# Optimization experiments

Hardware: AMD Instinct MI355X
Metric: run time of the kernel (lower is better)

Reference implementation:

```python
import jax, jax.numpy as jnp
import numpy as np

# Config mirroring the torch module's __init__ args
B = 2
LQ = 2048      # length_q
LKV = 2048     # length_kv
H = 8          # head_num
DQK = 64       # dim_QK
DV = 64        # dim_V
DIM_Q = 512
DIM_K = 512
DIM_VIN = 512
DIM_OUT = 512
SPAN = 64
STRIDE = 1


def setup_inputs() -> dict:
    key = jax.random.key(0)
    ks = jax.random.split(key, 7)
    s = 0.02  # small init scale for weights
    return {
        "q": jax.random.normal(ks[0], (B, LQ, DIM_Q), jnp.float32),
        "k": jax.random.normal(ks[1], (B, LKV, DIM_K), jnp.float32),
        "v": jax.random.normal(ks[2], (B, LKV, DIM_VIN), jnp.float32),
        "Wq": jax.random.normal(ks[3], (DIM_Q, H * DQK), jnp.float32) * s,
        "Wk": jax.random.normal(ks[4], (DIM_K, H * DQK), jnp.float32) * s,
        "Wv": jax.random.normal(ks[5], (DIM_VIN, H * DV), jnp.float32) * s,
        "Wout": jax.random.normal(ks[6], (H * DV, DIM_OUT), jnp.float32) * s,
    }


def reference(q, k, v, Wq, Wk, Wv, Wout):
    # Projections (torch nn.Linear without bias; weights stored as [in, out] here)
    Q = (q @ Wq).reshape(B, LQ, H, DQK)    # [B, Lq, H, DQK]
    K = (k @ Wk).reshape(B, LKV, H, DQK)   # [B, Lkv, H, DQK]
    V = (v @ Wv).reshape(B, LKV, H, DV)    # [B, Lkv, H, DV]

    # Window index table: for query t, key slot s attends kv position
    # kvi[s, t] = s - (SPAN-1) + STRIDE*t   (the conv1d-unfold in the original)
    s_idx = jnp.arange(SPAN)[:, None]
    t_idx = jnp.arange(LQ)[None, :]
    kvi = s_idx - (SPAN - 1) + STRIDE * t_idx          # [span, Lq]
    valid = (kvi >= 0) & (kvi < LKV)                   # [span, Lq]
    idx = jnp.clip(kvi, 0, LKV - 1)

    # Gather sliding windows (equivalent to conv_K/conv_V im2col tables)
    Kw = K[:, idx]   # [B, span, Lq, H, DQK]
    Vw = V[:, idx]   # [B, span, Lq, H, DV]

    scale = jnp.asarray(1.0 / np.sqrt(DQK), jnp.float32)
    scores = jnp.einsum('bthd,bsthd->bhst', Q, Kw) * scale   # [B, H, span, Lq]
    scores = jnp.where(valid[None, None], scores, -jnp.inf)
    p = jax.nn.softmax(scores, axis=2)                        # softmax over span

    o = jnp.einsum('bhst,bsthd->bthd', p, Vw).reshape(B, LQ, H * DV)
    return o @ Wout   # [B, Lq, dim_out]
```

## Files before the change

### kernel.cpp

```cpp
#include <hip/hip_runtime.h>

#define NB 2
#define SEQ 2048
#define NH 8
#define HD 64
#define DMODEL 512
#define WSPAN 64
#define MROWS (NB * SEQ)

typedef __attribute__((ext_vector_type(4))) float f32x4;
typedef __attribute__((ext_vector_type(4))) int i32x4;
typedef __attribute__((ext_vector_type(8))) short bf16x8;

static __device__ __forceinline__ float bf2f(unsigned short u) {
    return __uint_as_float(((unsigned int)u) << 16);
}
static __device__ __forceinline__ unsigned short f2bf(float f) {
    unsigned int x = __float_as_uint(f);
    x += 0x7fffu + ((x >> 16) & 1u);
    return (unsigned short)(x >> 16);
}

static __device__ __forceinline__ f32x4 mfma16(bf16x8 a, bf16x8 b, f32x4 c) {
    return __builtin_amdgcn_mfma_f32_16x16x32_bf16(a, b, c, 0, 0, 0);
}

struct Cvt3 {
    const float* src[3];
    unsigned short* dst[3];
};

__global__ __launch_bounds__(256) void cvt_big(Cvt3 a) {
    const int ai = blockIdx.y;
    const int idx = blockIdx.x * 256 + threadIdx.x;
    const float* s = a.src[ai] + (size_t)idx * 8;
    float4 f0 = *(const float4*)s;
    float4 f1 = *(const float4*)(s + 4);
    i32x4 o;
    o[0] = (int)((unsigned)f2bf(f0.x) | ((unsigned)f2bf(f0.y) << 16));
    o[1] = (int)((unsigned)f2bf(f0.z) | ((unsigned)f2bf(f0.w) << 16));
    o[2] = (int)((unsigned)f2bf(f1.x) | ((unsigned)f2bf(f1.y) << 16));
    o[3] = (int)((unsigned)f2bf(f1.z) | ((unsigned)f2bf(f1.w) << 16));
    *(i32x4*)(a.dst[ai] + (size_t)idx * 8) = o;
}

struct Wt4 {
    const float* src[4];
    unsigned short* dst[4];
};

__global__ __launch_bounds__(256) void cvt_wT(Wt4 a) {
    __shared__ unsigned short t64[64][72];
    const int w = blockIdx.z;
    const float* src = a.src[w];
    unsigned short* dst = a.dst[w];
    const int k0 = blockIdx.x * 64, n0 = blockIdx.y * 64;
    const int t = threadIdx.x;
    const int r = t >> 2;
    const int cg = (t & 3) * 16;
    const float* sp = src + (size_t)(k0 + r) * DMODEL + n0 + cg;
#pragma unroll
    for (int j = 0; j < 16; j += 4) {
        float4 f = *(const float4*)(sp + j);
        t64[r][cg + j + 0] = f2bf(f.x);
        t64[r][cg + j + 1] = f2bf(f.y);
        t64[r][cg + j + 2] = f2bf(f.z);
        t64[r][cg + j + 3] = f2bf(f.w);
    }
    __syncthreads();
    unsigned short buf[16];
#pragma unroll
    for (int j = 0; j < 16; ++j) buf[j] = t64[cg + j][r];
    unsigned short* dp = dst + (size_t)(n0 + r) * DMODEL + k0 + cg;
    *(i32x4*)dp = *(const i32x4*)buf;
    *(i32x4*)(dp + 8) = *(const i32x4*)(buf + 8);
}

#define TBM 128
#define TBN 128
#define TBK 32
#define LPAD 40

template <bool OUT_F32>
static __device__ __forceinline__ void gemm_core(const unsigned short* __restrict__ A,
                                                 const unsigned short* __restrict__ BT,
                                                 void* __restrict__ C, int m0, int n0) {
    constexpr int N = DMODEL, K = DMODEL;
    __shared__ __align__(16) unsigned short a_lds[TBM][LPAD];
    __shared__ __align__(16) unsigned short b_lds[TBN][LPAD];
    const int t = threadIdx.x;
    const int lane = t & 63;
    const int wv = t >> 6;
    const int s_r = t >> 1;
    const int s_k = (t & 1) * 16;
    const int fr = lane & 15;
    const int fk = (lane >> 4) * 8;
    const int wm = (wv & 1) * 64;
    const int wn = (wv >> 1) * 64;

    f32x4 acc[4][4];
#pragma unroll
    for (int i = 0; i < 4; ++i)
#pragma unroll
        for (int j = 0; j < 4; ++j) acc[i][j] = (f32x4){0.f, 0.f, 0.f, 0.f};

    for (int k0 = 0; k0 < K; k0 += TBK) {
        const unsigned short* ap = A + (size_t)(m0 + s_r) * K + k0 + s_k;
        const unsigned short* bp = BT + (size_t)(n0 + s_r) * K + k0 + s_k;
        i32x4 av0 = *(const i32x4*)ap;
        i32x4 av1 = *(const i32x4*)(ap + 8);
        i32x4 bv0 = *(const i32x4*)bp;
        i32x4 bv1 = *(const i32x4*)(bp + 8);
        __syncthreads();
        *(i32x4*)&a_lds[s_r][s_k] = av0;
        *(i32x4*)&a_lds[s_r][s_k + 8] = av1;
        *(i32x4*)&b_lds[s_r][s_k] = bv0;
        *(i32x4*)&b_lds[s_r][s_k + 8] = bv1;
        __syncthreads();
        bf16x8 af[4], bf[4];
#pragma unroll
        for (int i = 0; i < 4; ++i) {
            af[i] = *(const bf16x8*)&a_lds[wm + i * 16 + fr][fk];
            bf[i] = *(const bf16x8*)&b_lds[wn + i * 16 + fr][fk];
        }
#pragma unroll
        for (int mi = 0; mi < 4; ++mi)
#pragma unroll
            for (int ni = 0; ni < 4; ++ni) acc[mi][ni] = mfma16(af[mi], bf[ni], acc[mi][ni]);
    }
#pragma unroll
    for (int mi = 0; mi < 4; ++mi) {
#pragma unroll
        for (int ni = 0; ni < 4; ++ni) {
#pragma unroll
            for (int r = 0; r < 4; ++r) {
                const int row = m0 + wm + mi * 16 + (lane >> 4) * 4 + r;
                const int col = n0 + wn + ni * 16 + fr;
                if constexpr (OUT_F32)
                    ((float*)C)[(size_t)row * N + col] = acc[mi][ni][r];
                else
                    ((unsigned short*)C)[(size_t)row * N + col] = f2bf(acc[mi][ni][r]);
            }
        }
    }
}

__global__ __launch_bounds__(256) void gemm_proj(
    const unsigned short* __restrict__ qx, const unsigned short* __restrict__ kx,
    const unsigned short* __restrict__ vx, const unsigned short* __restrict__ wtq,
    const unsigned short* __restrict__ wtk, const unsigned short* __restrict__ wtv,
    unsigned short* __restrict__ Qp, unsigned short* __restrict__ Kp,
    unsigned short* __restrict__ Vp) {
    const unsigned short* A;
    const unsigned short* W;
    unsigned short* C;
    if (blockIdx.z == 0) { A = qx; W = wtq; C = Qp; }
    else if (blockIdx.z == 1) { A = kx; W = wtk; C = Kp; }
    else { A = vx; W = wtv; C = Vp; }
    gemm_core<false>(A, W, C, blockIdx.x * TBM, blockIdx.y * TBN);
}

__global__ __launch_bounds__(256) void gemm_out(const unsigned short* __restrict__ Op,
                                                const unsigned short* __restrict__ wto,
                                                float* __restrict__ out) {
    gemm_core<true>(Op, wto, out, blockIdx.x * TBM, blockIdx.y * TBN);
}

__global__ __launch_bounds__(256) void attn_win(const unsigned short* __restrict__ Qp,
                                                const unsigned short* __restrict__ Kp,
                                                const unsigned short* __restrict__ Vp,
                                                unsigned short* __restrict__ Op) {
    __shared__ __align__(16) unsigned short kt[128 * 64];
    __shared__ __align__(16) unsigned short vT[64 * 128];
    __shared__ __align__(16) unsigned short pw[4][16][104];
    const int tile = blockIdx.x, h = blockIdx.y, b = blockIdx.z;
    const int t0 = tile * 64;
    const int tid = threadIdx.x;
    const int lane = tid & 63;
    const int qg = tid >> 6;
    const int c = lane & 15;
    const int g = lane >> 4;
    const int hcol = h * HD;
    const size_t base = (size_t)b * SEQ * DMODEL;

    {
        const int l = tid >> 1;
        const int dh = (tid & 1) * 32;
        int j = t0 - (WSPAN - 1) + l;
        int jc = j < 0 ? 0 : (j > SEQ - 1 ? SEQ - 1 : j);
        const unsigned short* kp = Kp + base + (size_t)jc * DMODEL + hcol + dh;
        const unsigned short* vp = Vp + base + (size_t)jc * DMODEL + hcol + dh;
        const int lg = (l & 7) << 4;
#pragma unroll
        for (int u = 0; u < 4; ++u) {
            const int dg = dh + u * 8;
            i32x4 kv = *(const i32x4*)(kp + u * 8);
            i32x4 vv = *(const i32x4*)(vp + u * 8);
            *(i32x4*)((char*)kt + l * 128 + ((dg * 2) ^ lg)) = kv;
#pragma unroll
            for (int e2 = 0; e2 < 4; ++e2) {
                unsigned int w2 = (unsigned int)vv[e2];
                const int d0 = dg + 2 * e2, d1 = d0 + 1;
                *(unsigned short*)((char*)vT + d0 * 256 + ((((l >> 3) ^ (d0 & 15)) << 4)) +
                                   (l & 7) * 2) = (unsigned short)(w2 & 0xffffu);
                *(unsigned short*)((char*)vT + d1 * 256 + ((((l >> 3) ^ (d1 & 15)) << 4)) +
                                   (l & 7) * 2) = (unsigned short)(w2 >> 16);
            }
        }
    }
    *(unsigned long long*)&pw[qg][lane >> 2][80 + (lane & 3) * 4] = 0ull;
    __syncthreads();

    const unsigned short* qrow =
        Qp + base + (size_t)(t0 + 16 * qg + c) * DMODEL + hcol + 8 * g;
    const bf16x8 qa0 = *(const bf16x8*)qrow;
    const bf16x8 qa1 = *(const bf16x8*)(qrow + 32);
    f32x4 sacc[5];
#pragma unroll
    for (int kb = 0; kb < 5; ++kb) {
        sacc[kb] = (f32x4){0.f, 0.f, 0.f, 0.f};
        const int key = 16 * (qg + kb) + c;
        const int sw = (key & 7) << 4;
        bf16x8 kf0 = *(const bf16x8*)((const char*)kt + key * 128 + ((16 * g) ^ sw));
        bf16x8 kf1 = *(const bf16x8*)((const char*)kt + key * 128 + ((64 + 16 * g) ^ sw));
        sacc[kb] = mfma16(qa0, kf0, sacc[kb]);
        sacc[kb] = mfma16(qa1, kf1, sacc[kb]);
    }

    const int L0 = 63 - t0;
#pragma unroll
    for (int r = 0; r < 4; ++r) {
        const int iq = 4 * g + r;
        float sv[5];
        float m = -3e38f;
#pragma unroll
        for (int kb = 0; kb < 5; ++kb) {
            float x = sacc[kb][r] * 0.125f;
            const int dlk = 16 * kb + c - iq;
            const int l = 16 * (qg + kb) + c;
            x = (dlk >= 0 && dlk <= 63 && l >= L0) ? x : -3e38f;
            sv[kb] = x;
            m = fmaxf(m, x);
        }
#pragma unroll
        for (int off = 1; off <= 8; off <<= 1) m = fmaxf(m, __shfl_xor(m, off));
        float s = 0.f;
#pragma unroll
        for (int kb = 0; kb < 5; ++kb) {
            float pp = __expf(sv[kb] - m);
            sv[kb] = pp;
            s += pp;
        }
#pragma unroll
        for (int off = 1; off <= 8; off <<= 1) s += __shfl_xor(s, off);
        const float rinv = 1.0f / s;
#pragma unroll
        for (int kb = 0; kb < 5; ++kb)
            pw[qg][iq][16 * kb + c] = f2bf(sv[kb] * rinv);
    }

    f32x4 oacc[4];
#pragma unroll
    for (int nb = 0; nb < 4; ++nb) oacc[nb] = (f32x4){0.f, 0.f, 0.f, 0.f};
#pragma unroll
    for (int ks = 0; ks < 3; ++ks) {
        const bf16x8 pa = *(const bf16x8*)&pw[qg][c][ks * 32 + 8 * g];
        const int lbase = 16 * qg + ks * 32 + 8 * g;
        const int gran = ((lbase >> 3) & 15) ^ c;
#pragma unroll
        for (int nb = 0; nb < 4; ++nb) {
            const bf16x8 vf =
                *(const bf16x8*)((const char*)vT + (16 * nb + c) * 256 + (gran << 4));
            oacc[nb] = mfma16(pa, vf, oacc[nb]);
        }
    }

    unsigned short* orow = Op + base + (size_t)(t0 + 16 * qg + 4 * g) * DMODEL + hcol + c;
#pragma unroll
    for (int nb = 0; nb < 4; ++nb)
#pragma unroll
        for (int jr = 0; jr < 4; ++jr)
            orow[(size_t)jr * DMODEL + 16 * nb] = f2bf(oacc[nb][jr]);
}

extern "C" void kernel_launch(void* const* d_in, const int* in_sizes, int n_in,
                              void* d_out, int out_size, void* d_ws, size_t ws_size,
                              hipStream_t stream) {
    (void)in_sizes; (void)n_in; (void)out_size; (void)ws_size;
    const float* q = (const float*)d_in[0];
    const float* k = (const float*)d_in[1];
    const float* v = (const float*)d_in[2];
    const float* Wq = (const float*)d_in[3];
    const float* Wk = (const float*)d_in[4];
    const float* Wv = (const float*)d_in[5];
    const float* Wout = (const float*)d_in[6];

    const size_t NBIG = (size_t)MROWS * DMODEL;
    const size_t NW = (size_t)DMODEL * DMODEL;
    unsigned short* p = (unsigned short*)d_ws;
    unsigned short* qx = p;  p += NBIG;
    unsigned short* kx = p;  p += NBIG;
    unsigned short* vx = p;  p += NBIG;
    unsigned short* wtq = p; p += NW;
    unsigned short* wtk = p; p += NW;
    unsigned short* wtv = p; p += NW;
    unsigned short* wto = p; p += NW;
    unsigned short* Qp = p;  p += NBIG;
    unsigned short* Kp = p;  p += NBIG;
    unsigned short* Vp = p;  p += NBIG;
    unsigned short* Op = p;

    Cvt3 c3;
    c3.src[0] = q; c3.dst[0] = qx;
    c3.src[1] = k; c3.dst[1] = kx;
    c3.src[2] = v; c3.dst[2] = vx;
    Wt4 w4;
    w4.src[0] = Wq;   w4.dst[0] = wtq;
    w4.src[1] = Wk;   w4.dst[1] = wtk;
    w4.src[2] = Wv;   w4.dst[2] = wtv;
    w4.src[3] = Wout; w4.dst[3] = wto;

    cvt_big<<<dim3((unsigned)(NBIG / 8 / 256), 3), 256, 0, stream>>>(c3);
    cvt_wT<<<dim3(8, 8, 4), 256, 0, stream>>>(w4);
    gemm_proj<<<dim3(MROWS / TBM, DMODEL / TBN, 3), 256, 0, stream>>>(qx, kx, vx, wtq, wtk, wtv,
                                                                      Qp, Kp, Vp);
    attn_win<<<dim3(SEQ / 64, NH, NB), 256, 0, stream>>>(Qp, Kp, Vp, Op);
    gemm_out<<<dim3(MROWS / TBM, DMODEL / TBN), 256, 0, stream>>>(Op, wto, (float*)d_out);
}
```

Measured before the change: 121.1 us.

## Fuse fp32-to-bf16 input conversion into QKV GEMM and prefetch next K tile

Removes the separate cvt_big kernel and its bf16 intermediate buffers. The QKV projection GEMM now loads fp32 activations directly and packs them to bf16 in registers before staging them in LDS. The GEMM core also issues global loads for the next K tile before the MFMA work on the current one, a register-level software pipeline. The A operand is re-read as fp32 by every N-block (four column tiles), which doubles its global traffic compared with bf16 in exchange for one fewer launch and one fewer full round trip through memory.

```diff
diff --git a/kernel.cpp b/kernel.cpp
--- a/kernel.cpp
+++ b/kernel.cpp
@@ -20,28 +20,12 @@
     x += 0x7fffu + ((x >> 16) & 1u);
     return (unsigned short)(x >> 16);
 }
+static __device__ __forceinline__ int pk2(float x, float y) {
+    return (int)(((unsigned)f2bf(x)) | ((unsigned)f2bf(y) << 16));
+}
 
 static __device__ __forceinline__ f32x4 mfma16(bf16x8 a, bf16x8 b, f32x4 c) {
     return __builtin_amdgcn_mfma_f32_16x16x32_bf16(a, b, c, 0, 0, 0);
-}
-
-struct Cvt3 {
-    const float* src[3];
-    unsigned short* dst[3];
-};
-
-__global__ __launch_bounds__(256) void cvt_big(Cvt3 a) {
-    const int ai = blockIdx.y;
-    const int idx = blockIdx.x * 256 + threadIdx.x;
-    const float* s = a.src[ai] + (size_t)idx * 8;
-    float4 f0 = *(const float4*)s;
-    float4 f1 = *(const float4*)(s + 4);
-    i32x4 o;
-    o[0] = (int)((unsigned)f2bf(f0.x) | ((unsigned)f2bf(f0.y) << 16));
-    o[1] = (int)((unsigned)f2bf(f0.z) | ((unsigned)f2bf(f0.w) << 16));
-    o[2] = (int)((unsigned)f2bf(f1.x) | ((unsigned)f2bf(f1.y) << 16));
-    o[3] = (int)((unsigned)f2bf(f1.z) | ((unsigned)f2bf(f1.w) << 16));
-    *(i32x4*)(a.dst[ai] + (size_t)idx * 8) = o;
 }
 
 struct Wt4 {
@@ -81,11 +65,12 @@
 #define TBK 32
 #define LPAD 40
 
-template <bool OUT_F32>
-static __device__ __forceinline__ void gemm_core(const unsigned short* __restrict__ A,
+template <bool A_F32, bool OUT_F32>
+static __device__ __forceinline__ void gemm_core(const void* __restrict__ Av,
                                                  const unsigned short* __restrict__ BT,
                                                  void* __restrict__ C, int m0, int n0) {
     constexpr int N = DMODEL, K = DMODEL;
+    constexpr int NSTEP = K / TBK;
     __shared__ __align__(16) unsigned short a_lds[TBM][LPAD];
     __shared__ __align__(16) unsigned short b_lds[TBN][LPAD];
     const int t = threadIdx.x;
@@ -104,19 +89,37 @@
 #pragma unroll
         for (int j = 0; j < 4; ++j) acc[i][j] = (f32x4){0.f, 0.f, 0.f, 0.f};
 
-    for (int k0 = 0; k0 < K; k0 += TBK) {
-        const unsigned short* ap = A + (size_t)(m0 + s_r) * K + k0 + s_k;
+    i32x4 a0, a1, b0, b1;
+    auto load_ab = [&](int k0) {
+        if constexpr (A_F32) {
+            const float* ap = (const float*)Av + (size_t)(m0 + s_r) * K + k0 + s_k;
+            float4 f0 = *(const float4*)ap;
+            float4 f1 = *(const float4*)(ap + 4);
+            float4 f2 = *(const float4*)(ap + 8);
+            float4 f3 = *(const float4*)(ap + 12);
+            a0 = (i32x4){pk2(f0.x, f0.y), pk2(f0.z, f0.w), pk2(f1.x, f1.y), pk2(f1.z, f1.w)};
+            a1 = (i32x4){pk2(f2.x, f2.y), pk2(f2.z, f2.w), pk2(f3.x, f3.y), pk2(f3.z, f3.w)};
+        } else {
+            const unsigned short* ap =
+                (const unsigned short*)Av + (size_t)(m0 + s_r) * K + k0 + s_k;
+            a0 = *(const i32x4*)ap;
+            a1 = *(const i32x4*)(ap + 8);
+        }
         const unsigned short* bp = BT + (size_t)(n0 + s_r) * K + k0 + s_k;
-        i32x4 av0 = *(const i32x4*)ap;
-        i32x4 av1 = *(const i32x4*)(ap + 8);
-        i32x4 bv0 = *(const i32x4*)bp;
-        i32x4 bv1 = *(const i32x4*)(bp + 8);
+        b0 = *(const i32x4*)bp;
+        b1 = *(const i32x4*)(bp + 8);
+    };
+
+    load_ab(0);
+    for (int ks = 0; ks < NSTEP; ++ks) {
         __syncthreads();
-        *(i32x4*)&a_lds[s_r][s_k] = av0;
-        *(i32x4*)&a_lds[s_r][s_k + 8] = av1;
-        *(i32x4*)&b_lds[s_r][s_k] = bv0;
-        *(i32x4*)&b_lds[s_r][s_k + 8] = bv1;
+        *(i32x4*)&a_lds[s_r][s_k] = a0;
+        *(i32x4*)&a_lds[s_r][s_k + 8] = a1;
+        *(i32x4*)&b_lds[s_r][s_k] = b0;
+        *(i32x4*)&b_lds[s_r][s_k + 8] = b1;
         __syncthreads();
+        const int kn = (ks + 1 < NSTEP) ? (ks + 1) * TBK : ks * TBK;
+        load_ab(kn);
         bf16x8 af[4], bf[4];
 #pragma unroll
         for (int i = 0; i < 4; ++i) {
@@ -145,25 +148,24 @@
     }
 }
 
-__global__ __launch_bounds__(256) void gemm_proj(
-    const unsigned short* __restrict__ qx, const unsigned short* __restrict__ kx,
-    const unsigned short* __restrict__ vx, const unsigned short* __restrict__ wtq,
-    const unsigned short* __restrict__ wtk, const unsigned short* __restrict__ wtv,
-    unsigned short* __restrict__ Qp, unsigned short* __restrict__ Kp,
-    unsigned short* __restrict__ Vp) {
-    const unsigned short* A;
+__global__ __launch_bounds__(256) void gemm_qkv(
+    const float* __restrict__ q, const float* __restrict__ k, const float* __restrict__ v,
+    const unsigned short* __restrict__ wtq, const unsigned short* __restrict__ wtk,
+    const unsigned short* __restrict__ wtv, unsigned short* __restrict__ Qp,
+    unsigned short* __restrict__ Kp, unsigned short* __restrict__ Vp) {
+    const float* A;
     const unsigned short* W;
     unsigned short* C;
-    if (blockIdx.z == 0) { A = qx; W = wtq; C = Qp; }
-    else if (blockIdx.z == 1) { A = kx; W = wtk; C = Kp; }
-    else { A = vx; W = wtv; C = Vp; }
-    gemm_core<false>(A, W, C, blockIdx.x * TBM, blockIdx.y * TBN);
+    if (blockIdx.z == 0) { A = q; W = wtq; C = Qp; }
+    else if (blockIdx.z == 1) { A = k; W = wtk; C = Kp; }
+    else { A = v; W = wtv; C = Vp; }
+    gemm_core<true, false>(A, W, C, blockIdx.x * TBM, blockIdx.y * TBN);
 }
 
 __global__ __launch_bounds__(256) void gemm_out(const unsigned short* __restrict__ Op,
                                                 const unsigned short* __restrict__ wto,
                                                 float* __restrict__ out) {
-    gemm_core<true>(Op, wto, out, blockIdx.x * TBM, blockIdx.y * TBN);
+    gemm_core<false, true>(Op, wto, out, blockIdx.x * TBM, blockIdx.y * TBN);
 }
 
 __global__ __launch_bounds__(256) void attn_win(const unsigned short* __restrict__ Qp,
@@ -298,9 +300,6 @@
     const size_t NBIG = (size_t)MROWS * DMODEL;
     const size_t NW = (size_t)DMODEL * DMODEL;
     unsigned short* p = (unsigned short*)d_ws;
-    unsigned short* qx = p;  p += NBIG;
-    unsigned short* kx = p;  p += NBIG;
-    unsigned short* vx = p;  p += NBIG;
     unsigned short* wtq = p; p += NW;
     unsigned short* wtk = p; p += NW;
     unsigned short* wtv = p; p += NW;
@@ -310,20 +309,15 @@
     unsigned short* Vp = p;  p += NBIG;
     unsigned short* Op = p;
 
-    Cvt3 c3;
-    c3.src[0] = q; c3.dst[0] = qx;
-    c3.src[1] = k; c3.dst[1] = kx;
-    c3.src[2] = v; c3.dst[2] = vx;
     Wt4 w4;
     w4.src[0] = Wq;   w4.dst[0] = wtq;
     w4.src[1] = Wk;   w4.dst[1] = wtk;
     w4.src[2] = Wv;   w4.dst[2] = wtv;
     w4.src[3] = Wout; w4.dst[3] = wto;
 
-    cvt_big<<<dim3((unsigned)(NBIG / 8 / 256), 3), 256, 0, stream>>>(c3);
     cvt_wT<<<dim3(8, 8, 4), 256, 0, stream>>>(w4);
-    gemm_proj<<<dim3(MROWS / TBM, DMODEL / TBN, 3), 256, 0, stream>>>(qx, kx, vx, wtq, wtk, wtv,
-                                                                      Qp, Kp, Vp);
+    gemm_qkv<<<dim3(MROWS / TBM, DMODEL / TBN, 3), 256, 0, stream>>>(q, k, v, wtq, wtk, wtv,
+                                                                     Qp, Kp, Vp);
     attn_win<<<dim3(SEQ / 64, NH, NB), 256, 0, stream>>>(Qp, Kp, Vp, Op);
     gemm_out<<<dim3(MROWS / TBM, DMODEL / TBN), 256, 0, stream>>>(Op, wto, (float*)d_out);
 }
```

Measured after the change: 117.0 us. -3.4%, faster.
